# Kernel tuning notes

Measured on AMD Instinct MI355X. Metric: run time of the kernel, lower is better.

Reference implementation:

```python
import jax, jax.numpy as jnp
import numpy as np

DIM = 1024
HEAD_DIM = 64
N_HEADS = DIM // HEAD_DIM  # 16
COND_DIM = 256
LENGTHS = (1, 4, 16, 64, 256, 1024)
SEQ = sum(LENGTHS)  # 1365
LN_EPS = 1e-5
ROT_D = 3 * (HEAD_DIM // 8)  # 24; 2*ROT_D = 48 <= HEAD_DIM


def _axial_pos(h, w):
    hp = np.linspace(-1.0, 1.0, h + 1); hp = (hp[:-1] + hp[1:]) / 2
    wp = np.linspace(-1.0, 1.0, w + 1); wp = (wp[:-1] + wp[1:]) / 2
    return np.stack(np.meshgrid(hp, wp, indexing='ij'), -1).reshape(h * w, 2)


def _make_theta():
    d = 5
    poses = []
    for i in range(d):
        pa = _axial_pos(32 >> i, 32 >> i)
        pr = np.full((pa.shape[0], 1), (d - i) / d)
        poses.insert(0, np.concatenate([pa, pr], -1))
    poses.insert(0, np.zeros((1, 3)))
    pos = np.concatenate(poses, 0)  # [1365, 3]
    log_min, log_max = np.log(np.pi), np.log(10 * np.pi)
    freqs = np.exp(np.linspace(log_min, log_max, HEAD_DIM // 8 * N_HEADS + 1)[:-1])
    freqs = freqs.reshape(HEAD_DIM // 8, N_HEADS).T  # [H, head_dim//8]
    th = pos[:, None, 0:1] * freqs  # [S, H, head_dim//8]
    tw = pos[:, None, 1:2] * freqs
    td = pos[:, None, 2:3] * freqs
    theta = np.concatenate([th, tw, td], -1)  # [S, H, ROT_D]
    return jnp.asarray(theta.transpose(1, 0, 2), dtype=jnp.float32)  # [H, S, ROT_D]


def _make_mask():
    m = np.zeros((SEQ, SEQ), dtype=bool)
    i = 0
    for L in LENGTHS:
        m[i:, i:i + L] = True
        i += L
    return jnp.asarray(m)


THETA = _make_theta()  # [H, S, ROT_D], constant buffer
MASK = _make_mask()    # [S, S] bool, constant buffer


def _rope(x, theta):
    # x: [B, H, S, head_dim]; theta: [H, S, ROT_D]
    d = theta.shape[-1]
    x1, x2, rest = x[..., :d], x[..., d:2 * d], x[..., 2 * d:]
    cos, sin = jnp.cos(theta), jnp.sin(theta)
    return jnp.concatenate([x1 * cos - x2 * sin, x2 * cos + x1 * sin, rest], -1)


def setup_inputs() -> dict:
    key = jax.random.key(0)
    ks = jax.random.split(key, 6)
    s = 0.02
    x = jax.random.normal(ks[0], (8, SEQ, DIM), jnp.float32)
    cond = jax.random.normal(ks[1], (8, 1, COND_DIM), jnp.float32)
    adaln_w = jax.random.normal(ks[2], (COND_DIM, 2 * DIM), jnp.float32) * s
    adaln_b = jnp.zeros((2 * DIM,), jnp.float32)
    qkv_w = jax.random.normal(ks[3], (DIM, 3 * DIM), jnp.float32) * s
    qkv_b = jnp.zeros((3 * DIM,), jnp.float32)
    out_w = jax.random.normal(ks[4], (DIM, DIM), jnp.float32) * s
    out_b = jnp.zeros((DIM,), jnp.float32)
    return {"x": x, "cond": cond, "adaln_w": adaln_w, "adaln_b": adaln_b,
            "qkv_w": qkv_w, "qkv_b": qkv_b, "out_w": out_w, "out_b": out_b}


def reference(x, cond, adaln_w, adaln_b, qkv_w, qkv_b, out_w, out_b):
    B, S, _ = x.shape
    skip = x
    # AdaLN: zero-init proj in the original; math is LN(x)*(w+1)+b
    wb = cond @ adaln_w + adaln_b  # [B, 1, 2*DIM]
    w, b = jnp.split(wb, 2, axis=-1)
    mu = x.mean(-1, keepdims=True)
    var = ((x - mu) ** 2).mean(-1, keepdims=True)
    xn = (x - mu) * jax.lax.rsqrt(var + LN_EPS)
    xn = xn * (w + 1.0) + b
    # QKV
    qkv = xn @ qkv_w + qkv_b  # [B, S, 3*DIM]
    qkv = qkv.reshape(B, S, 3, N_HEADS, HEAD_DIM).transpose(0, 3, 2, 1, 4)  # [B,H,3,S,hd]
    q, k, v = qkv[:, :, 0], qkv[:, :, 1], qkv[:, :, 2]
    theta = THETA[:, :S]  # [H, S, ROT_D]
    q = _rope(q, theta)
    k = _rope(k, theta)
    # block-causal masked SDPA
    scores = jnp.einsum('bhqd,bhkd->bhqk', q, k) / np.sqrt(HEAD_DIM).astype(np.float32)
    scores = jnp.where(MASK[:S, :S], scores, -1e30)
    attn = jax.nn.softmax(scores, axis=-1)
    o = jnp.einsum('bhqk,bhkd->bhqd', attn, v)
    o = o.transpose(0, 2, 1, 3).reshape(B, S, DIM)
    return o @ out_w + out_b + skip
```

## Files before the change

### kernel.cpp

```cpp
#include <hip/hip_runtime.h>
#include <math.h>


typedef unsigned short u16;
typedef unsigned short u16x8 __attribute__((ext_vector_type(8)));
typedef unsigned short u16x4 __attribute__((ext_vector_type(4)));
typedef __bf16        bf16x8 __attribute__((ext_vector_type(8)));
typedef float         f32x4  __attribute__((ext_vector_type(4)));

#define SEQ  1365
#define SP   1408
#define BHN  128
#define MTOT 10920
#define DIMN 1024
#define QSCALE 0.1803368801111204f

__device__ __forceinline__ u16 f2bf(float x){
  unsigned r; asm("v_cvt_pk_bf16_f32 %0, %1, %1" : "=v"(r) : "v"(x));
  return (u16)r;
}
__device__ __forceinline__ unsigned cvtpk(float a, float b){
  unsigned r; asm("v_cvt_pk_bf16_f32 %0, %1, %2" : "=v"(r) : "v"(a), "v"(b));
  return r;
}
__device__ __forceinline__ float bf2f(u16 b){
  return __builtin_bit_cast(float, ((unsigned)b) << 16);
}
__device__ __forceinline__ bf16x8 ldbf8(const u16* p){
  return __builtin_bit_cast(bf16x8, *(const u16x8*)p);
}
__device__ __forceinline__ bf16x8 ldsv(const char* p){
  return __builtin_bit_cast(bf16x8, *(const u16x8*)p);
}
__device__ __forceinline__ f32x4 mfma16(bf16x8 a, bf16x8 b, f32x4 c){
  return __builtin_amdgcn_mfma_f32_16x16x32_bf16(a, b, c, 0, 0, 0);
}
__device__ __forceinline__ void gload16(const u16* g, u16* l){
  __builtin_amdgcn_global_load_lds(
      (const __attribute__((address_space(1))) void*)(g),
      (__attribute__((address_space(3))) void*)(l), 16, 0, 0);
}

__global__ __launch_bounds__(256) void transpose_bf16(const float* __restrict__ in,
                                                      u16* __restrict__ outT,
                                                      int K, int N){
  __shared__ float tile[32][33];
  const int tx = threadIdx.x & 31, ty = threadIdx.x >> 5;
  const int n0 = blockIdx.x*32, k0 = blockIdx.y*32;
#pragma unroll
  for (int i=0;i<32;i+=8) tile[ty+i][tx] = in[(size_t)(k0+ty+i)*N + n0+tx];
  __syncthreads();
#pragma unroll
  for (int i=0;i<32;i+=8) outT[(size_t)(n0+ty+i)*K + k0+tx] = f2bf(tile[tx][ty+i]);
}

__global__ __launch_bounds__(256) void adaln_kernel(const float* __restrict__ cond,
                                                    const float* __restrict__ w,
                                                    const float* __restrict__ bsrc,
                                                    float* __restrict__ wb){
  __shared__ float cs[256];
  const int bt = blockIdx.x >> 3, ch = blockIdx.x & 7;
  const int t = threadIdx.x;
  cs[t] = cond[bt*256 + t];
  __syncthreads();
  const int n = ch*256 + t;
  float acc = bsrc[n];
  for (int j=0;j<256;j++) acc += cs[j] * w[(size_t)j*2048 + n];
  wb[bt*2048 + n] = acc;
}

__global__ __launch_bounds__(256) void theta_kernel(float* __restrict__ ctab,
                                                    float* __restrict__ stab){
  int idx = blockIdx.x*256 + threadIdx.x;
  if (idx >= 16*SEQ*24) return;
  int c = idx % 24;
  int rest = idx / 24;
  int s = rest % SEQ;
  int h = rest / SEQ;
  float p0 = 0.f, p1 = 0.f, p2 = 0.f;
  if (s >= 1){
    int start, sh; float pr;
    if      (s <   5){start=1;   sh=1; pr=0.2f;}
    else if (s <  21){start=5;   sh=2; pr=0.4f;}
    else if (s <  85){start=21;  sh=3; pr=0.6f;}
    else if (s < 341){start=85;  sh=4; pr=0.8f;}
    else             {start=341; sh=5; pr=1.0f;}
    int n = s - start;
    int row = n >> sh, colp = n & ((1<<sh)-1);
    float g = (float)(1 << sh);
    p0 = -1.f + (2*row+1)/g;
    p1 = -1.f + (2*colp+1)/g;
    p2 = pr;
  }
  int j = c & 7, comp = c >> 3;
  float kf = (float)(j*16 + h);
  float freq = 3.14159265358979323846f * exp2f(kf * (3.3219280948873623f/128.f));
  float pos = (comp==0) ? p0 : ((comp==1) ? p1 : p2);
  float th = pos * freq;
  ctab[idx] = cosf(th);
  stab[idx] = sinf(th);
}

__global__ __launch_bounds__(256) void ln_kernel(const float* __restrict__ x,
                                                 const float* __restrict__ wb,
                                                 u16* __restrict__ xn){
  const int row = blockIdx.x;
  const int b = row / SEQ;
  const int t = threadIdx.x, w = t>>6, l = t&63;
  const float4 v = ((const float4*)(x + (size_t)row*DIMN))[t];
  float s = v.x + v.y + v.z + v.w;
#pragma unroll
  for (int m=1; m<64; m<<=1) s += __shfl_xor(s, m);
  __shared__ float red1[4], red2[4];
  if (l == 0) red1[w] = s;
  __syncthreads();
  float mean = (red1[0]+red1[1]+red1[2]+red1[3]) * (1.f/1024.f);
  float dx = v.x-mean, dy = v.y-mean, dz = v.z-mean, dw = v.w-mean;
  float q = dx*dx + dy*dy + dz*dz + dw*dw;
#pragma unroll
  for (int m=1; m<64; m<<=1) q += __shfl_xor(q, m);
  if (l == 0) red2[w] = q;
  __syncthreads();
  float var = (red2[0]+red2[1]+red2[2]+red2[3]) * (1.f/1024.f);
  float rs = rsqrtf(var + 1e-5f);
  const float* wrow = wb + b*2048;
  int n0 = t*4;
  u16x4 o;
  o[0] = f2bf(dx*rs*(wrow[n0+0]+1.f) + wrow[1024+n0+0]);
  o[1] = f2bf(dy*rs*(wrow[n0+1]+1.f) + wrow[1024+n0+1]);
  o[2] = f2bf(dz*rs*(wrow[n0+2]+1.f) + wrow[1024+n0+2]);
  o[3] = f2bf(dw*rs*(wrow[n0+3]+1.f) + wrow[1024+n0+3]);
  *(u16x4*)&xn[(size_t)row*DIMN + n0] = o;
}

#define GSTAGE(dstA, dstB, koff)                                   \
  do {                                                             \
    _Pragma("unroll")                                              \
    for (int j_=0;j_<4;j_++) gload16(sA[j_]+(koff), (dstA)+j_*512);\
    _Pragma("unroll")                                              \
    for (int j_=0;j_<4;j_++) gload16(sB[j_]+(koff), (dstB)+j_*512);\
  } while(0)

__global__ __launch_bounds__(256, 2) void gemm_qkv(const u16* __restrict__ A,
                                                   const u16* __restrict__ BT,
                                                   const float* __restrict__ bias,
                                                   u16* __restrict__ qb, u16* __restrict__ kb,
                                                   u16* __restrict__ vb){
  __shared__ u16 SMEM[32768];
  u16* As0 = SMEM;        u16* As1 = SMEM + 8192;
  u16* Bs0 = SMEM + 16384; u16* Bs1 = SMEM + 24576;
  const int t = threadIdx.x, l = t & 63, w = t >> 6;
  const int lr = l & 15, lg = l >> 4;
  const int wr = w >> 1, wc = w & 1;

  const int bid = blockIdx.x;
  const int wg = (bid & 7)*264 + (bid >> 3);
  const int stile = wg/96, rr = wg - stile*96;
  const int mt = stile*4 + rr/24, nt = rr - (rr/24)*24;
  const int bat = mt / 11, mtl = mt - bat*11;
  const int s0 = mtl*128;
  const int bn = nt*128;

  const int row8 = l >> 3;
  const int gch  = (l & 7) ^ row8;
  const u16* sA[4]; const u16* sB[4];
#pragma unroll
  for (int j=0;j<4;j++){
    int srow = s0 + w*32 + j*8 + row8; if (srow > SEQ-1) srow = SEQ-1;
    sA[j] = A  + ((size_t)(bat*SEQ + srow))*1024 + gch*8;
    sB[j] = BT + (size_t)(bn + w*32 + j*8 + row8)*1024 + gch*8;
  }
  u16* dA0 = &As0[w*2048]; u16* dB0 = &Bs0[w*2048];
  u16* dA1 = &As1[w*2048]; u16* dB1 = &Bs1[w*2048];

  const int pch  = (lg ^ (lr & 7)) << 4;
  const int aoff = (wr*64 + lr)*128 + pch;
  const int boff = (wc*64 + lr)*128 + pch;

  f32x4 acc[4][4];
#pragma unroll
  for (int mi=0;mi<4;mi++)
#pragma unroll
    for (int ni=0;ni<4;ni++) acc[mi][ni] = (f32x4){0.f,0.f,0.f,0.f};

  GSTAGE(dA0, dB0, 0);
  GSTAGE(dA1, dB1, 64);
  asm volatile("s_waitcnt vmcnt(8)" ::: "memory");
  __builtin_amdgcn_s_barrier();
  __builtin_amdgcn_sched_barrier(0);

  for (int kt = 0; kt < 16; ++kt){
    const int bi = kt & 1;
    const char* Ab = (const char*)(bi ? As1 : As0);
    const char* Bb = (const char*)(bi ? Bs1 : Bs0);
    u16* dA = bi ? dA1 : dA0;
    u16* dB = bi ? dB1 : dB0;
    bf16x8 a0[4], b0[4], a1[4], b1[4];
#pragma unroll
    for (int mi=0;mi<4;mi++) a0[mi] = ldsv(Ab + (aoff + mi*2048));
#pragma unroll
    for (int ni=0;ni<4;ni++) b0[ni] = ldsv(Bb + (boff + ni*2048));
#pragma unroll
    for (int mi=0;mi<4;mi++) a1[mi] = ldsv(Ab + ((aoff + mi*2048) ^ 64));
#pragma unroll
    for (int ni=0;ni<4;ni++) b1[ni] = ldsv(Bb + ((boff + ni*2048) ^ 64));
    __builtin_amdgcn_s_setprio(1);
#pragma unroll
    for (int mi=0;mi<4;mi++)
#pragma unroll
      for (int ni=0;ni<4;ni++)
        acc[mi][ni] = mfma16(a0[mi], b0[ni], acc[mi][ni]);
    __builtin_amdgcn_s_setprio(0);
    asm volatile("s_waitcnt lgkmcnt(0)" ::: "memory");
    __builtin_amdgcn_s_barrier();
    __builtin_amdgcn_sched_barrier(0);
    if (kt < 14) GSTAGE(dA, dB, (kt+2)*64);
    __builtin_amdgcn_sched_barrier(0);
    __builtin_amdgcn_s_setprio(1);
#pragma unroll
    for (int mi=0;mi<4;mi++)
#pragma unroll
      for (int ni=0;ni<4;ni++)
        acc[mi][ni] = mfma16(a1[mi], b1[ni], acc[mi][ni]);
    __builtin_amdgcn_s_setprio(0);
    if (kt < 15){
      if (kt < 14) asm volatile("s_waitcnt vmcnt(8)" ::: "memory");
      else         asm volatile("s_waitcnt vmcnt(0)" ::: "memory");
      __builtin_amdgcn_s_barrier();
      __builtin_amdgcn_sched_barrier(0);
    }
  }

  __syncthreads();
  const int three = bn >> 10;
  const int hb = (bn & 1023) >> 6;
  if (three < 2){
    const float scl = (three==0) ? QSCALE : 1.0f;
#pragma unroll
    for (int mi=0;mi<4;mi++)
#pragma unroll
      for (int ni=0;ni<4;ni++){
        int col = wc*64 + ni*16 + lr;
        float bia = bias[bn + col];
#pragma unroll
        for (int r=0;r<4;r++){
          int ml = wr*64 + mi*16 + lg*4 + r;
          SMEM[ml*136 + col] = f2bf((acc[mi][ni][r] + bia) * scl);
        }
      }
    __syncthreads();
    u16* dst = (three==0) ? qb : kb;
    const int cs = t & 15, tm = t >> 4;
    const int h = hb + (cs>>3), d8 = (cs&7)*8;
#pragma unroll
    for (int p=0;p<8;p++){
      int ml = p*16 + tm;
      int s = s0 + ml;
      u16x8 vv = *(const u16x8*)&SMEM[ml*136 + cs*8];
      if (s < SEQ)
        *(u16x8*)&dst[((size_t)(bat*16 + h)*SP + s)*64 + d8] = vv;
    }
  } else {
#pragma unroll
    for (int mi=0;mi<4;mi++)
#pragma unroll
      for (int ni=0;ni<4;ni++){
        int col = wc*64 + ni*16 + lr;
        float bia = bias[bn + col];
#pragma unroll
        for (int r=0;r<4;r+=2){
          int ml = wr*64 + mi*16 + lg*4 + r;
          *(unsigned*)&SMEM[col*136 + ml] = cvtpk(acc[mi][ni][r]+bia, acc[mi][ni][r+1]+bia);
        }
      }
    __syncthreads();
    const int ss = t & 15, tdl = t >> 4;
    if (s0 + 127 < SEQ){
#pragma unroll
      for (int p=0;p<8;p++){
        int dl = p*16 + tdl;
        int h = hb + (dl>>6), d = dl & 63;
        u16x8 vv = *(const u16x8*)&SMEM[dl*136 + ss*8];
        *(u16x8*)&vb[((size_t)(bat*16 + h)*64 + d)*SP + s0 + ss*8] = vv;
      }
    } else {
#pragma unroll
      for (int p=0;p<8;p++){
        int dl = p*16 + tdl;
        int h = hb + (dl>>6), d = dl & 63;
        size_t rowb = ((size_t)(bat*16 + h)*64 + d)*SP;
#pragma unroll
        for (int j=0;j<8;j++){
          int s = s0 + ss*8 + j;
          if (s < SEQ) vb[rowb + s] = SMEM[dl*136 + ss*8 + j];
        }
      }
    }
  }
}

__global__ __launch_bounds__(256) void rope2_kernel(u16* __restrict__ qb,
                                                    u16* __restrict__ kb,
                                                    const float* __restrict__ ctab,
                                                    const float* __restrict__ stab){
  int rid = blockIdx.x*256 + threadIdx.x;
  if (rid >= BHN*SEQ) return;
  int bh = rid / SEQ, s = rid - bh*SEQ, h = bh & 15;
  const float* cp = ctab + (size_t)(h*SEQ + s)*24;
  const float* sp = stab + (size_t)(h*SEQ + s)*24;
  float cs[24], sn[24];
#pragma unroll
  for (int i=0;i<6;i++){
    ((float4*)cs)[i] = ((const float4*)cp)[i];
    ((float4*)sn)[i] = ((const float4*)sp)[i];
  }
  size_t base = ((size_t)bh*SP + s)*64;
  u16 buf[48];
#pragma unroll
  for (int i=0;i<6;i++) ((u16x8*)buf)[i] = *(const u16x8*)&qb[base + i*8];
#pragma unroll
  for (int j=0;j<24;j++){
    float x1 = bf2f(buf[j]), x2 = bf2f(buf[24+j]);
    buf[j]    = f2bf(x1*cs[j] - x2*sn[j]);
    buf[24+j] = f2bf(x2*cs[j] + x1*sn[j]);
  }
#pragma unroll
  for (int i=0;i<6;i++) *(u16x8*)&qb[base + i*8] = ((u16x8*)buf)[i];
#pragma unroll
  for (int i=0;i<6;i++) ((u16x8*)buf)[i] = *(const u16x8*)&kb[base + i*8];
#pragma unroll
  for (int j=0;j<24;j++){
    float x1 = bf2f(buf[j]), x2 = bf2f(buf[24+j]);
    buf[j]    = f2bf(x1*cs[j] - x2*sn[j]);
    buf[24+j] = f2bf(x2*cs[j] + x1*sn[j]);
  }
#pragma unroll
  for (int i=0;i<6;i++) *(u16x8*)&kb[base + i*8] = ((u16x8*)buf)[i];
}

__global__ __launch_bounds__(256, 3) void attn_kernel(const u16* __restrict__ qb,
                                                      const u16* __restrict__ kb,
                                                      const u16* __restrict__ vb,
                                                      u16* __restrict__ ob){
  __shared__ u16 Ks[2][4096];
  __shared__ u16 Vs[2][4096];
  __shared__ u16 Ps[128*72];
  const int bx = blockIdx.x;
  const int qt = (bx < 9) ? (bx + 2) : (bx - 9);
  const int bh = blockIdx.y;
  const int t = threadIdx.x, w = t>>6, l = t&63, lr = l&15, lg = l>>4, lg4 = lg<<2;
  const u16* qB = qb + (size_t)bh*SP*64;
  const u16* kB = kb + (size_t)bh*SP*64;
  const u16* vB = vb + (size_t)bh*64*SP;
  const int q0 = qt*128 + w*32;

  bf16x8 qf[2][2];
#pragma unroll
  for (int ni=0; ni<2; ni++)
#pragma unroll
    for (int kk=0; kk<2; kk++)
      qf[ni][kk] = ldbf8(&qB[(size_t)(q0+ni*16+lr)*64 + kk*32 + lg*8]);
  const int qg0 = q0 + lr, qg1 = q0 + 16 + lr;

  const int row8 = l >> 3;
  const int gch  = (l & 7) ^ row8;
  const u16* sK[2]; const u16* sV[2];
#pragma unroll
  for (int j=0;j<2;j++){
    sK[j] = kB + (size_t)(w*16 + j*8 + row8)*64 + gch*8;
    sV[j] = vB + (size_t)(w*16 + j*8 + row8)*SP + gch*8;
  }
  const int sw0 = ((lg)   ^ (lr & 7)) << 4;
  const int sw1 = ((4+lg) ^ (lr & 7)) << 4;

#define KVSTAGE(buf_, kb_)                                          \
  do {                                                              \
    _Pragma("unroll")                                               \
    for (int j_=0;j_<2;j_++){                                       \
      gload16(sK[j_] + (kb_)*64, &Ks[buf_][(w*16+j_*8)*64]);        \
      gload16(sV[j_] + (kb_),    &Vs[buf_][(w*16+j_*8)*64]);        \
    }                                                               \
  } while(0)

  f32x4 oacc[2][4];
#pragma unroll
  for (int mo=0;mo<2;mo++)
#pragma unroll
    for (int nd=0;nd<4;nd++) oacc[mo][nd] = (f32x4){0.f,0.f,0.f,0.f};
  float lst[2] = {0.f, 0.f};

  int qmax = min(qt*128+127, SEQ-1);
  int kend = (qmax<1)?1:(qmax<5)?5:(qmax<21)?21:(qmax<85)?85:(qmax<341)?341:SEQ;
  int nkt = (kend + 63) >> 6;

  KVSTAGE(0, 0);
  KVSTAGE(1, 64);

  for (int kt=0; kt<nkt; kt++){
    const int kbase = kt*64;
    const int cur = kt & 1;
    asm volatile("s_waitcnt vmcnt(4)" ::: "memory");
    __builtin_amdgcn_s_barrier();
    __builtin_amdgcn_sched_barrier(0);
    const char* Kb = (const char*)&Ks[cur][0];
    const char* Vb = (const char*)&Vs[cur][0];

    f32x4 sacc[4][2];
#pragma unroll
    for (int mi=0;mi<4;mi++){
      sacc[mi][0] = (f32x4){0.f,0.f,0.f,0.f};
      sacc[mi][1] = (f32x4){0.f,0.f,0.f,0.f};
    }
#pragma unroll
    for (int mi=0;mi<4;mi++){
      bf16x8 k0f = ldsv(Kb + (mi*16+lr)*128 + sw0);
      bf16x8 k1f = ldsv(Kb + (mi*16+lr)*128 + sw1);
      sacc[mi][0] = mfma16(k0f, qf[0][0], sacc[mi][0]);
      sacc[mi][0] = mfma16(k1f, qf[0][1], sacc[mi][0]);
      sacc[mi][1] = mfma16(k0f, qf[1][0], sacc[mi][1]);
      sacc[mi][1] = mfma16(k1f, qf[1][1], sacc[mi][1]);
    }

    int lastk = kbase + 63;
    int visLast = (lastk>=SEQ)?(1<<30):(lastk>=341)?341:(lastk>=85)?85:
                  (lastk>=21)?21:(lastk>=5)?5:(lastk>=1)?1:0;
    if (visLast > q0){
#pragma unroll
      for (int mi=0;mi<4;mi++){
        int kv = kbase + mi*16 + lg4;
#pragma unroll
        for (int r=0;r<4;r++){
          int key = kv + r;
          int visv = (key>=SEQ)?(1<<30):(key>=341)?341:(key>=85)?85:
                     (key>=21)?21:(key>=5)?5:(key>=1)?1:0;
          if (qg0 < visv) sacc[mi][0][r] = -1e30f;
          if (qg1 < visv) sacc[mi][1][r] = -1e30f;
        }
      }
    }

    float pa[2] = {0.f, 0.f}, pb[2] = {0.f, 0.f};
#pragma unroll
    for (int mi=0;mi<4;mi++)
#pragma unroll
      for (int ni=0;ni<2;ni++){
        float p0 = __builtin_amdgcn_exp2f(sacc[mi][ni][0]);
        float p1 = __builtin_amdgcn_exp2f(sacc[mi][ni][1]);
        float p2 = __builtin_amdgcn_exp2f(sacc[mi][ni][2]);
        float p3 = __builtin_amdgcn_exp2f(sacc[mi][ni][3]);
        pa[ni] += p0 + p1;
        pb[ni] += p2 + p3;
        uint2 pk = { cvtpk(p0, p1), cvtpk(p2, p3) };
        *(uint2*)&Ps[(w*32+ni*16+lr)*72 + mi*16 + lg4] = pk;
      }
#pragma unroll
    for (int ni=0;ni<2;ni++){
      float s = pa[ni] + pb[ni];
      s += __shfl_xor(s, 16);
      s += __shfl_xor(s, 32);
      lst[ni] += s;
    }

    bf16x8 pf[2][2];
#pragma unroll
    for (int mo=0;mo<2;mo++)
#pragma unroll
      for (int kk=0;kk<2;kk++)
        pf[mo][kk] = ldbf8(&Ps[(w*32+mo*16+lr)*72 + kk*32 + lg*8]);
#pragma unroll
    for (int nd=0;nd<4;nd++){
      bf16x8 v0 = ldsv(Vb + (nd*16+lr)*128 + sw0);
      bf16x8 v1 = ldsv(Vb + (nd*16+lr)*128 + sw1);
#pragma unroll
      for (int mo=0;mo<2;mo++){
        oacc[mo][nd] = mfma16(pf[mo][0], v0, oacc[mo][nd]);
        oacc[mo][nd] = mfma16(pf[mo][1], v1, oacc[mo][nd]);
      }
    }

    asm volatile("s_waitcnt lgkmcnt(0)" ::: "memory");
    __builtin_amdgcn_s_barrier();
    __builtin_amdgcn_sched_barrier(0);
    if (kt < nkt-1){
      int kpf = (kt+2 < nkt ? kt+2 : nkt-1)*64;
      KVSTAGE(cur, kpf);
    }
    __builtin_amdgcn_sched_barrier(0);
  }

  const int b = bh >> 4, h = bh & 15;
  float linv[2][4];
#pragma unroll
  for (int mo=0;mo<2;mo++)
#pragma unroll
    for (int r=0;r<4;r++)
      linv[mo][r] = 1.f / __shfl(lst[mo], lg4 + r);
#pragma unroll
  for (int mo=0;mo<2;mo++)
#pragma unroll
    for (int r=0;r<4;r++){
      int p = q0 + mo*16 + lg4 + r;
      if (p < SEQ){
#pragma unroll
        for (int nd=0;nd<4;nd++)
          ob[((size_t)(b*SEQ + p))*DIMN + h*64 + nd*16 + lr] = f2bf(oacc[mo][nd][r] * linv[mo][r]);
      }
    }
#undef KVSTAGE
}

__global__ __launch_bounds__(256, 2) void gemm_out(const u16* __restrict__ A,
                                                   const u16* __restrict__ BT,
                                                   const float* __restrict__ bias,
                                                   const float* __restrict__ skip,
                                                   float* __restrict__ out){
  __shared__ u16 SMEM[32768];
  u16* As0 = SMEM;        u16* As1 = SMEM + 8192;
  u16* Bs0 = SMEM + 16384; u16* Bs1 = SMEM + 24576;
  const int t = threadIdx.x, l = t & 63, w = t >> 6;
  const int lr = l & 15, lg = l >> 4;
  const int wr = w >> 1, wc = w & 1;

  const int bid = blockIdx.x;
  const int wg = (bid & 7)*88 + (bid >> 3);
  const int stile = wg/32, rr = wg & 31;
  const int mt = stile*4 + rr/8, nt = rr & 7;
  const int bat = mt / 11, mtl = mt - bat*11;
  const int s0 = mtl*128;
  const int bn = nt*128;

  const int row8 = l >> 3;
  const int gch  = (l & 7) ^ row8;
  const u16* sA[4]; const u16* sB[4];
#pragma unroll
  for (int j=0;j<4;j++){
    int srow = s0 + w*32 + j*8 + row8; if (srow > SEQ-1) srow = SEQ-1;
    sA[j] = A  + ((size_t)(bat*SEQ + srow))*1024 + gch*8;
    sB[j] = BT + (size_t)(bn + w*32 + j*8 + row8)*1024 + gch*8;
  }
  u16* dA0 = &As0[w*2048]; u16* dB0 = &Bs0[w*2048];
  u16* dA1 = &As1[w*2048]; u16* dB1 = &Bs1[w*2048];

  const int pch  = (lg ^ (lr & 7)) << 4;
  const int aoff = (wr*64 + lr)*128 + pch;
  const int boff = (wc*64 + lr)*128 + pch;

  f32x4 acc[4][4];
#pragma unroll
  for (int mi=0;mi<4;mi++)
#pragma unroll
    for (int ni=0;ni<4;ni++) acc[mi][ni] = (f32x4){0.f,0.f,0.f,0.f};

  GSTAGE(dA0, dB0, 0);
  GSTAGE(dA1, dB1, 64);
  asm volatile("s_waitcnt vmcnt(8)" ::: "memory");
  __builtin_amdgcn_s_barrier();
  __builtin_amdgcn_sched_barrier(0);

  for (int kt = 0; kt < 16; ++kt){
    const int bi = kt & 1;
    const char* Ab = (const char*)(bi ? As1 : As0);
    const char* Bb = (const char*)(bi ? Bs1 : Bs0);
    u16* dA = bi ? dA1 : dA0;
    u16* dB = bi ? dB1 : dB0;
    bf16x8 a0[4], b0[4], a1[4], b1[4];
#pragma unroll
    for (int mi=0;mi<4;mi++) a0[mi] = ldsv(Ab + (aoff + mi*2048));
#pragma unroll
    for (int ni=0;ni<4;ni++) b0[ni] = ldsv(Bb + (boff + ni*2048));
#pragma unroll
    for (int mi=0;mi<4;mi++) a1[mi] = ldsv(Ab + ((aoff + mi*2048) ^ 64));
#pragma unroll
    for (int ni=0;ni<4;ni++) b1[ni] = ldsv(Bb + ((boff + ni*2048) ^ 64));
    __builtin_amdgcn_s_setprio(1);
#pragma unroll
    for (int mi=0;mi<4;mi++)
#pragma unroll
      for (int ni=0;ni<4;ni++)
        acc[mi][ni] = mfma16(a0[mi], b0[ni], acc[mi][ni]);
    __builtin_amdgcn_s_setprio(0);
    asm volatile("s_waitcnt lgkmcnt(0)" ::: "memory");
    __builtin_amdgcn_s_barrier();
    __builtin_amdgcn_sched_barrier(0);
    if (kt < 14) GSTAGE(dA, dB, (kt+2)*64);
    __builtin_amdgcn_sched_barrier(0);
    __builtin_amdgcn_s_setprio(1);
#pragma unroll
    for (int mi=0;mi<4;mi++)
#pragma unroll
      for (int ni=0;ni<4;ni++)
        acc[mi][ni] = mfma16(a1[mi], b1[ni], acc[mi][ni]);
    __builtin_amdgcn_s_setprio(0);
    if (kt < 15){
      if (kt < 14) asm volatile("s_waitcnt vmcnt(8)" ::: "memory");
      else         asm volatile("s_waitcnt vmcnt(0)" ::: "memory");
      __builtin_amdgcn_s_barrier();
      __builtin_amdgcn_sched_barrier(0);
    }
  }

  __syncthreads();
  float* Lf = (float*)SMEM;
#pragma unroll
  for (int mi=0;mi<4;mi++)
#pragma unroll
    for (int ni=0;ni<4;ni++){
      int col = wc*64 + ni*16 + lr;
      float bia = bias[bn + col];
#pragma unroll
      for (int r=0;r<4;r++){
        int ml = wr*64 + mi*16 + lg*4 + r;
        Lf[ml*128 + col] = acc[mi][ni][r] + bia;
      }
    }
  __syncthreads();
  const int cs = t & 31, tm = t >> 5;
#pragma unroll
  for (int p=0;p<16;p++){
    int ml = p*8 + tm;
    int s = s0 + ml;
    if (s < SEQ){
      size_t idx2 = (size_t)(bat*SEQ + s)*1024 + bn + cs*4;
      float4 v4 = *(const float4*)&Lf[ml*128 + cs*4];
      const float4 sk = *(const float4*)&skip[idx2];
      float4 o4; o4.x=v4.x+sk.x; o4.y=v4.y+sk.y; o4.z=v4.z+sk.z; o4.w=v4.w+sk.w;
      *(float4*)&out[idx2] = o4;
    }
  }
}

extern "C" void kernel_launch(void* const* d_in, const int* in_sizes, int n_in,
                              void* d_out, int out_size, void* d_ws, size_t ws_size,
                              hipStream_t stream) {
  (void)in_sizes; (void)n_in; (void)out_size; (void)ws_size;
  const float* x        = (const float*)d_in[0];
  const float* cond     = (const float*)d_in[1];
  const float* adaln_w  = (const float*)d_in[2];
  const float* adaln_b  = (const float*)d_in[3];
  const float* qkv_w    = (const float*)d_in[4];
  const float* qkv_b    = (const float*)d_in[5];
  const float* out_w    = (const float*)d_in[6];
  const float* out_b    = (const float*)d_in[7];
  float* out = (float*)d_out;

  char* ws = (char*)d_ws;
  size_t off = 0;
  auto alloc = [&](size_t bytes)->void*{
    void* p = ws + off;
    off += (bytes + 255) & ~(size_t)255;
    return p;
  };
  float* wb     = (float*)alloc((size_t)8*2048*4);
  u16*   xn     = (u16*)  alloc((size_t)MTOT*DIMN*2);
  u16*   qkv_wT = (u16*)  alloc((size_t)3072*1024*2);
  u16*   out_wT = (u16*)  alloc((size_t)1024*1024*2);
  u16*   qbuf   = (u16*)  alloc((size_t)BHN*SP*64*2);
  u16*   kbuf   = (u16*)  alloc((size_t)BHN*SP*64*2);
  u16*   vbuf   = (u16*)  alloc((size_t)BHN*SP*64*2);
  float* ctab   = (float*)alloc((size_t)16*SEQ*24*4);
  float* stab   = (float*)alloc((size_t)16*SEQ*24*4);
  u16*   obuf   = xn;

  transpose_bf16<<<dim3(3072/32, 1024/32), 256, 0, stream>>>(qkv_w, qkv_wT, 1024, 3072);
  transpose_bf16<<<dim3(1024/32, 1024/32), 256, 0, stream>>>(out_w, out_wT, 1024, 1024);
  theta_kernel<<<(16*SEQ*24 + 255)/256, 256, 0, stream>>>(ctab, stab);
  adaln_kernel<<<64, 256, 0, stream>>>(cond, adaln_w, adaln_b, wb);
  ln_kernel<<<MTOT, 256, 0, stream>>>(x, wb, xn);
  gemm_qkv<<<2112, 256, 0, stream>>>(xn, qkv_wT, qkv_b, qbuf, kbuf, vbuf);
  rope2_kernel<<<(BHN*SEQ + 255)/256, 256, 0, stream>>>(qbuf, kbuf, ctab, stab);
  attn_kernel<<<dim3((SEQ+127)/128, BHN), 256, 0, stream>>>(qbuf, kbuf, vbuf, obuf);
  gemm_out<<<704, 256, 0, stream>>>(obuf, out_wT, out_b, x, out);
}
```

Measured before the change: 371.0 us.

## Switch attention to 32x32x16 MFMA and keep P in registers

```diff
diff --git a/kernel.cpp b/kernel.cpp
--- a/kernel.cpp
+++ b/kernel.cpp
@@ -5,8 +5,10 @@
 typedef unsigned short u16;
 typedef unsigned short u16x8 __attribute__((ext_vector_type(8)));
 typedef unsigned short u16x4 __attribute__((ext_vector_type(4)));
+typedef unsigned int   u32x4 __attribute__((ext_vector_type(4)));
 typedef __bf16        bf16x8 __attribute__((ext_vector_type(8)));
 typedef float         f32x4  __attribute__((ext_vector_type(4)));
+typedef float         f32x16 __attribute__((ext_vector_type(16)));
 
 #define SEQ  1365
 #define SP   1408
@@ -34,6 +36,9 @@
 }
 __device__ __forceinline__ f32x4 mfma16(bf16x8 a, bf16x8 b, f32x4 c){
   return __builtin_amdgcn_mfma_f32_16x16x32_bf16(a, b, c, 0, 0, 0);
+}
+__device__ __forceinline__ f32x16 mfma32(bf16x8 a, bf16x8 b, f32x16 c){
+  return __builtin_amdgcn_mfma_f32_32x32x16_bf16(a, b, c, 0, 0, 0);
 }
 __device__ __forceinline__ void gload16(const u16* g, u16* l){
   __builtin_amdgcn_global_load_lds(
@@ -344,23 +349,24 @@
                                                       u16* __restrict__ ob){
   __shared__ u16 Ks[2][4096];
   __shared__ u16 Vs[2][4096];
-  __shared__ u16 Ps[128*72];
   const int bx = blockIdx.x;
   const int qt = (bx < 9) ? (bx + 2) : (bx - 9);
   const int bh = blockIdx.y;
-  const int t = threadIdx.x, w = t>>6, l = t&63, lr = l&15, lg = l>>4, lg4 = lg<<2;
+  const int t = threadIdx.x, w = t>>6, l = t&63;
+  const int lo = l & 31, hi = l >> 5;
   const u16* qB = qb + (size_t)bh*SP*64;
   const u16* kB = kb + (size_t)bh*SP*64;
   const u16* vB = vb + (size_t)bh*64*SP;
   const int q0 = qt*128 + w*32;
 
-  bf16x8 qf[2][2];
-#pragma unroll
-  for (int ni=0; ni<2; ni++)
-#pragma unroll
-    for (int kk=0; kk<2; kk++)
-      qf[ni][kk] = ldbf8(&qB[(size_t)(q0+ni*16+lr)*64 + kk*32 + lg*8]);
-  const int qg0 = q0 + lr, qg1 = q0 + 16 + lr;
+  bf16x8 qf[4];
+  {
+    int qr = q0 + lo; if (qr > SEQ-1) qr = SEQ-1;
+#pragma unroll
+    for (int c=0;c<4;c++)
+      qf[c] = ldbf8(&qB[(size_t)qr*64 + c*16 + hi*8]);
+  }
+  const int qg = q0 + lo;
 
   const int row8 = l >> 3;
   const int gch  = (l & 7) ^ row8;
@@ -370,8 +376,7 @@
     sK[j] = kB + (size_t)(w*16 + j*8 + row8)*64 + gch*8;
     sV[j] = vB + (size_t)(w*16 + j*8 + row8)*SP + gch*8;
   }
-  const int sw0 = ((lg)   ^ (lr & 7)) << 4;
-  const int sw1 = ((4+lg) ^ (lr & 7)) << 4;
+  const int lom = lo & 7;
 
 #define KVSTAGE(buf_, kb_)                                          \
   do {                                                              \
@@ -382,12 +387,12 @@
     }                                                               \
   } while(0)
 
-  f32x4 oacc[2][4];
-#pragma unroll
-  for (int mo=0;mo<2;mo++)
-#pragma unroll
-    for (int nd=0;nd<4;nd++) oacc[mo][nd] = (f32x4){0.f,0.f,0.f,0.f};
-  float lst[2] = {0.f, 0.f};
+  f32x16 oacc[2];
+#pragma unroll
+  for (int vbk=0;vbk<2;vbk++)
+#pragma unroll
+    for (int r=0;r<16;r++) oacc[vbk][r] = 0.f;
+  float lst = 0.f;
 
   int qmax = min(qt*128+127, SEQ-1);
   int kend = (qmax<1)?1:(qmax<5)?5:(qmax<21)?21:(qmax<85)?85:(qmax<341)?341:SEQ;
@@ -405,78 +410,73 @@
     const char* Kb = (const char*)&Ks[cur][0];
     const char* Vb = (const char*)&Vs[cur][0];
 
-    f32x4 sacc[4][2];
-#pragma unroll
-    for (int mi=0;mi<4;mi++){
-      sacc[mi][0] = (f32x4){0.f,0.f,0.f,0.f};
-      sacc[mi][1] = (f32x4){0.f,0.f,0.f,0.f};
-    }
-#pragma unroll
-    for (int mi=0;mi<4;mi++){
-      bf16x8 k0f = ldsv(Kb + (mi*16+lr)*128 + sw0);
-      bf16x8 k1f = ldsv(Kb + (mi*16+lr)*128 + sw1);
-      sacc[mi][0] = mfma16(k0f, qf[0][0], sacc[mi][0]);
-      sacc[mi][0] = mfma16(k1f, qf[0][1], sacc[mi][0]);
-      sacc[mi][1] = mfma16(k0f, qf[1][0], sacc[mi][1]);
-      sacc[mi][1] = mfma16(k1f, qf[1][1], sacc[mi][1]);
-    }
+    f32x16 sacc[2];
+#pragma unroll
+    for (int kbk=0;kbk<2;kbk++)
+#pragma unroll
+      for (int r=0;r<16;r++) sacc[kbk][r] = 0.f;
+#pragma unroll
+    for (int kbk=0;kbk<2;kbk++)
+#pragma unroll
+      for (int c=0;c<4;c++){
+        int pch = ((2*c + hi) ^ lom) << 4;
+        bf16x8 kf = ldsv(Kb + (kbk*32+lo)*128 + pch);
+        sacc[kbk] = mfma32(kf, qf[c], sacc[kbk]);
+      }
 
     int lastk = kbase + 63;
     int visLast = (lastk>=SEQ)?(1<<30):(lastk>=341)?341:(lastk>=85)?85:
                   (lastk>=21)?21:(lastk>=5)?5:(lastk>=1)?1:0;
     if (visLast > q0){
 #pragma unroll
-      for (int mi=0;mi<4;mi++){
-        int kv = kbase + mi*16 + lg4;
-#pragma unroll
-        for (int r=0;r<4;r++){
-          int key = kv + r;
+      for (int kbk=0;kbk<2;kbk++)
+#pragma unroll
+        for (int r=0;r<16;r++){
+          int key = kbase + kbk*32 + (r&3) + 8*(r>>2) + 4*hi;
           int visv = (key>=SEQ)?(1<<30):(key>=341)?341:(key>=85)?85:
                      (key>=21)?21:(key>=5)?5:(key>=1)?1:0;
-          if (qg0 < visv) sacc[mi][0][r] = -1e30f;
-          if (qg1 < visv) sacc[mi][1][r] = -1e30f;
+          if (qg < visv) sacc[kbk][r] = -1e30f;
         }
-      }
-    }
-
-    float pa[2] = {0.f, 0.f}, pb[2] = {0.f, 0.f};
-#pragma unroll
-    for (int mi=0;mi<4;mi++)
-#pragma unroll
-      for (int ni=0;ni<2;ni++){
-        float p0 = __builtin_amdgcn_exp2f(sacc[mi][ni][0]);
-        float p1 = __builtin_amdgcn_exp2f(sacc[mi][ni][1]);
-        float p2 = __builtin_amdgcn_exp2f(sacc[mi][ni][2]);
-        float p3 = __builtin_amdgcn_exp2f(sacc[mi][ni][3]);
-        pa[ni] += p0 + p1;
-        pb[ni] += p2 + p3;
-        uint2 pk = { cvtpk(p0, p1), cvtpk(p2, p3) };
-        *(uint2*)&Ps[(w*32+ni*16+lr)*72 + mi*16 + lg4] = pk;
-      }
-#pragma unroll
-    for (int ni=0;ni<2;ni++){
-      float s = pa[ni] + pb[ni];
-      s += __shfl_xor(s, 16);
-      s += __shfl_xor(s, 32);
-      lst[ni] += s;
-    }
-
-    bf16x8 pf[2][2];
-#pragma unroll
-    for (int mo=0;mo<2;mo++)
-#pragma unroll
-      for (int kk=0;kk<2;kk++)
-        pf[mo][kk] = ldbf8(&Ps[(w*32+mo*16+lr)*72 + kk*32 + lg*8]);
-#pragma unroll
-    for (int nd=0;nd<4;nd++){
-      bf16x8 v0 = ldsv(Vb + (nd*16+lr)*128 + sw0);
-      bf16x8 v1 = ldsv(Vb + (nd*16+lr)*128 + sw1);
-#pragma unroll
-      for (int mo=0;mo<2;mo++){
-        oacc[mo][nd] = mfma16(pf[mo][0], v0, oacc[mo][nd]);
-        oacc[mo][nd] = mfma16(pf[mo][1], v1, oacc[mo][nd]);
-      }
-    }
+    }
+
+    float psum = 0.f;
+    bf16x8 pafv[4];
+#pragma unroll
+    for (int kbk=0;kbk<2;kbk++){
+      float p[16];
+#pragma unroll
+      for (int r=0;r<16;r++){
+        p[r] = __builtin_amdgcn_exp2f(sacc[kbk][r]);
+        psum += p[r];
+      }
+#pragma unroll
+      for (int e=0;e<2;e++){
+        unsigned w0 = cvtpk(p[8*e+0], p[8*e+1]);
+        unsigned w1 = cvtpk(p[8*e+2], p[8*e+3]);
+        unsigned w2 = cvtpk(p[8*e+4], p[8*e+5]);
+        unsigned w3 = cvtpk(p[8*e+6], p[8*e+7]);
+        unsigned sw0 = (unsigned)__shfl_xor((int)w0, 32);
+        unsigned sw1 = (unsigned)__shfl_xor((int)w1, 32);
+        unsigned sw2 = (unsigned)__shfl_xor((int)w2, 32);
+        unsigned sw3 = (unsigned)__shfl_xor((int)w3, 32);
+        unsigned A0 = hi ? sw2 : w0;
+        unsigned A1 = hi ? sw3 : w1;
+        unsigned A2 = hi ? w2  : sw0;
+        unsigned A3 = hi ? w3  : sw1;
+        pafv[kbk*2+e] = __builtin_bit_cast(bf16x8, (u32x4){A0, A1, A2, A3});
+      }
+    }
+    psum += __shfl_xor(psum, 32);
+    lst += psum;
+
+#pragma unroll
+    for (int vbk=0;vbk<2;vbk++)
+#pragma unroll
+      for (int kc=0;kc<4;kc++){
+        int pch = ((2*kc + hi) ^ lom) << 4;
+        bf16x8 vf = ldsv(Vb + (vbk*32+lo)*128 + pch);
+        oacc[vbk] = mfma32(pafv[kc], vf, oacc[vbk]);
+      }
 
     asm volatile("s_waitcnt lgkmcnt(0)" ::: "memory");
     __builtin_amdgcn_s_barrier();
@@ -489,23 +489,18 @@
   }
 
   const int b = bh >> 4, h = bh & 15;
-  float linv[2][4];
-#pragma unroll
-  for (int mo=0;mo<2;mo++)
-#pragma unroll
-    for (int r=0;r<4;r++)
-      linv[mo][r] = 1.f / __shfl(lst[mo], lg4 + r);
-#pragma unroll
-  for (int mo=0;mo<2;mo++)
-#pragma unroll
-    for (int r=0;r<4;r++){
-      int p = q0 + mo*16 + lg4 + r;
-      if (p < SEQ){
-#pragma unroll
-        for (int nd=0;nd<4;nd++)
-          ob[((size_t)(b*SEQ + p))*DIMN + h*64 + nd*16 + lr] = f2bf(oacc[mo][nd][r] * linv[mo][r]);
-      }
-    }
+#pragma unroll
+  for (int r=0;r<16;r++){
+    int qloc = (r&3) + 8*(r>>2) + 4*hi;
+    float Ls = __shfl(lst, qloc);
+    float linv = 1.f / Ls;
+    int p = q0 + qloc;
+    if (p < SEQ){
+      size_t rowb = ((size_t)(b*SEQ + p))*DIMN + h*64 + lo;
+      ob[rowb]      = f2bf(oacc[0][r] * linv);
+      ob[rowb + 32] = f2bf(oacc[1][r] * linv);
+    }
+  }
 #undef KVSTAGE
 }
 
@@ -668,6 +663,6 @@
   ln_kernel<<<MTOT, 256, 0, stream>>>(x, wb, xn);
   gemm_qkv<<<2112, 256, 0, stream>>>(xn, qkv_wT, qkv_b, qbuf, kbuf, vbuf);
   rope2_kernel<<<(BHN*SEQ + 255)/256, 256, 0, stream>>>(qbuf, kbuf, ctab, stab);
-  attn_kernel<<<dim3((SEQ+127)/128, BHN), 256, 0, stream>>>(qbuf, kbuf, vbuf, obuf);
+  attn_kernel<<<dim3(11, BHN), 256, 0, stream>>>(qbuf, kbuf, vbuf, obuf);
   gemm_out<<<704, 256, 0, stream>>>(obuf, out_wT, out_b, x, out);
 }
```

After: 387.0 us. +4.3%, slower.
